# Optimization experiments

Hardware: AMD Instinct MI355X
Metric: run time of the kernel (lower is better)

Reference implementation:

```python
import jax, jax.numpy as jnp
import numpy as np

B = 1024           # number of jets (independent binary trees)
L = 10             # tree depth (levels); level j has B*2**j nodes
H = 128            # hidden size
FEAT = 7           # input features per node
LEVEL_SIZES = [B * 2**j for j in range(L)]
OFF = np.concatenate([[0], np.cumsum(LEVEL_SIZES)]).astype(int).tolist()
INNER = LEVEL_SIZES[:-1]                     # all non-bottom nodes are inner
COFF = np.concatenate([[0], np.cumsum(INNER)]).astype(int).tolist()


def _linear_init(key, fan_in, fan_out):
    return jax.random.normal(key, (fan_in, fan_out), jnp.float32) / np.sqrt(fan_in).astype(np.float32)


def setup_inputs() -> dict:
    key = jax.random.key(0)
    ks = jax.random.split(key, 6)
    contents = jax.random.normal(ks[0], (OFF[-1], FEAT), jnp.float32)
    # child indices are local to level j+1: node k at level j -> children (2k, 2k+1)
    ch = [np.stack([2 * np.arange(n), 2 * np.arange(n) + 1], axis=1) for n in INNER]
    children = jnp.asarray(np.concatenate(ch, axis=0), jnp.int32)
    return {
        "contents": contents,
        "children": children,
        "W_u": _linear_init(ks[1], FEAT, H), "b_u": jnp.zeros((H,), jnp.float32),
        "W_h": _linear_init(ks[2], 3 * H, H), "b_h": jnp.zeros((H,), jnp.float32),
        "W_z": _linear_init(ks[3], 4 * H, 4 * H), "b_z": jnp.zeros((4 * H,), jnp.float32),
        "W_r": _linear_init(ks[4], 3 * H, 3 * H), "b_r": jnp.zeros((3 * H,), jnp.float32),
        "conv_w": jnp.asarray([0.9], jnp.float32),
        "conv_b": jnp.asarray([0.01], jnp.float32),
    }


def reference(contents, children, W_u, b_u, W_h, b_h, W_z, b_z, W_r, b_r, conv_w, conv_b):
    def conv_chain(x):
        # relu(conv1x1(relu(conv1x1(relu(conv1x1(x)))))): Conv2d(1,1,1) == scalar scale + bias
        for _ in range(3):
            x = jax.nn.relu(conv_w[0] * x + conv_b[0])
        return x

    emb = None  # embeddings of the level below (level j+1)
    for j in reversed(range(L)):
        c = contents[OFF[j]:OFF[j + 1]]               # [N_j, FEAT]
        u = conv_chain(c @ W_u + b_u)                 # [N_j, H]
        if j == L - 1:                                # bottom level: all leaves
            emb = u
            continue
        ch = children[COFF[j]:COFF[j + 1]]            # [N_j, 2] indices into level j+1
        h_L = emb[ch[:, 0]]                           # gather left children
        h_R = emb[ch[:, 1]]                           # gather right children
        hhu = jnp.concatenate([h_L, h_R, u], axis=1)  # [N_j, 3H]
        r = jax.nn.sigmoid(hhu @ W_r + b_r)           # reset gate
        h_H = conv_chain((r * hhu) @ W_h + b_h)       # [N_j, H]
        z = jnp.concatenate([h_H, hhu], axis=1) @ W_z + b_z  # [N_j, 4H]
        g = jax.nn.softmax(
            jnp.stack([z[:, :H], z[:, H:2 * H], z[:, 2 * H:3 * H], z[:, 3 * H:]], axis=-1),
            axis=-1,
        )                                             # [N_j, H, 4] gate weights
        emb = g[..., 0] * h_H + g[..., 1] * h_L + g[..., 2] * h_R + g[..., 3] * u
    return emb.reshape(B, -1)                         # [B, H] root embeddings
```

## Files before the change

kernel.cpp:

```cpp
#include <hip/hip_runtime.h>
#include <hip/hip_bf16.h>

typedef _Float16 f16x8 __attribute__((ext_vector_type(8)));
typedef _Float16 f16x4 __attribute__((ext_vector_type(4)));
typedef float f32x4 __attribute__((ext_vector_type(4)));

#define H 128
#define FEAT 7
#define RB 64
#define NT 512

__device__ __forceinline__ float conv3(float x, float w, float b) {
    x = fmaxf(fmaf(w, x, b), 0.f);
    x = fmaxf(fmaf(w, x, b), 0.f);
    x = fmaxf(fmaf(w, x, b), 0.f);
    return x;
}
__device__ __forceinline__ float sigm(float x) {
    return __builtin_amdgcn_rcpf(1.f + __expf(-x));
}

__global__ __launch_bounds__(256) void pack_weights(
    const float* __restrict__ Wu, const float* __restrict__ Wr,
    const float* __restrict__ Wh, const float* __restrict__ Wz,
    _Float16* __restrict__ Pu, _Float16* __restrict__ Pr,
    _Float16* __restrict__ Ph, _Float16* __restrict__ Pz)
{
    int idx = blockIdx.x * 256 + threadIdx.x;
    if (idx < 384 * 384) {
        int k = idx / 384, n = idx % 384;
        Pr[((size_t)(k >> 3) * 384 + n) * 8 + (k & 7)] = (_Float16)Wr[idx];
    }
    if (idx < 384 * 128) {
        int k = idx / 128, n = idx % 128;
        Ph[((size_t)(k >> 3) * 128 + n) * 8 + (k & 7)] = (_Float16)Wh[idx];
    }
    if (idx < 512 * 512) {
        int k = idx / 512, n = idx % 512;
        Pz[((size_t)(k >> 3) * 512 + n) * 8 + (k & 7)] = (_Float16)Wz[idx];
    }
    if (idx < 128 * 32) {
        int n = idx & 127, kk = idx >> 7;
        Pu[((size_t)(kk >> 3) * 128 + n) * 8 + (kk & 7)] =
            (kk < FEAT) ? (_Float16)Wu[kk * H + n] : (_Float16)0.f;
    }
}

template<bool LEAF>
__global__ __launch_bounds__(NT, 2) void level_kernel(
    const float* __restrict__ contents,
    const int* __restrict__ children,
    const float* __restrict__ leafContents,
    const _Float16* __restrict__ embPrev,
    _Float16* __restrict__ embOut,
    float* __restrict__ finalOut,
    const _Float16* __restrict__ Pu, const float* __restrict__ bu,
    const _Float16* __restrict__ Pr, const float* __restrict__ br,
    const _Float16* __restrict__ Ph, const float* __restrict__ bh,
    const _Float16* __restrict__ Pz, const float* __restrict__ bz,
    const float* __restrict__ convw, const float* __restrict__ convb)
{
    __shared__ __align__(16) _Float16 s_hhu[RB][392];
    __shared__ __align__(16) _Float16 s_x[RB][392];
    __shared__ __align__(16) _Float16 s_hH[RB][136];

    const int t = threadIdx.x;
    const int row0 = blockIdx.x * RB;
    const float cw = convw[0], cbv = convb[0];

    const int lane = t & 63;
    const int w = t >> 6;
    const int q = lane >> 4;
    const int ln = lane & 15;

    const f16x8* PBc = (const f16x8*)Pr + (w * 48 + ln);
    f16x8 awc[3][3];
#pragma unroll
    for (int c = 0; c < 3; c++) awc[0][c] = PBc[(size_t)q * 384 + c * 16];
#pragma unroll
    for (int c = 0; c < 3; c++) awc[1][c] = PBc[(size_t)(4 + q) * 384 + c * 16];

    _Float16* wbuf = (_Float16*)&s_x[0][0];
    {
        int r = t >> 3, k = t & 7;
        wbuf[t] = (k < FEAT) ? (_Float16)contents[(size_t)(row0 + r) * FEAT + k]
                             : (_Float16)0.f;
        if (LEAF) {
            int base = children[row0 * 2];
            const float* lc = leafContents + (size_t)base * FEAT;
#pragma unroll
            for (int p = 0; p < 2; p++) {
                int e = p * 512 + t;
                int r2 = e >> 3, k2 = e & 7;
                wbuf[512 + e] = (k2 < FEAT) ? (_Float16)lc[(size_t)r2 * FEAT + k2]
                                            : (_Float16)0.f;
            }
        } else {
            int rp = t >> 4, chunk = t & 15;
#pragma unroll
            for (int p = 0; p < 4; p++) {
                int cr = p * 32 + rp;
                int child = children[row0 * 2 + cr];
                uint4 v = *(const uint4*)(embPrev + (size_t)child * H + chunk * 8);
                *(uint4*)&s_hhu[cr >> 1][(cr & 1) * 128 + chunk * 8] = v;
            }
        }
    }
    __syncthreads();

    {
        f16x8 puF = ((const f16x8*)Pu)[(size_t)q * 128 + w * 16 + ln];
        const int fb = w * 16 + q * 4;
        f32x4 buv = *(const f32x4*)&bu[fb];
        {
            f16x8 bA[4];
#pragma unroll
            for (int rt = 0; rt < 4; rt++)
                bA[rt] = *(const f16x8*)&wbuf[(rt * 16 + ln) * 8];
            f32x4 accA[4];
#pragma unroll
            for (int rt = 0; rt < 4; rt++)
                accA[rt] = __builtin_amdgcn_mfma_f32_16x16x32_f16(puF, bA[rt], (f32x4){0,0,0,0}, 0, 0, 0);
#pragma unroll
            for (int rt = 0; rt < 4; rt++) {
                f16x4 hp;
#pragma unroll
                for (int reg = 0; reg < 4; reg++)
                    hp[reg] = (_Float16)conv3(accA[rt][reg] + buv[reg], cw, cbv);
                *(f16x4*)&s_hhu[rt * 16 + ln][256 + fb] = hp;
            }
        }
        if (LEAF) {
#pragma unroll
            for (int h = 0; h < 2; h++) {
                f16x8 bB[4];
#pragma unroll
                for (int rt = 0; rt < 4; rt++)
                    bB[rt] = *(const f16x8*)&wbuf[512 + ((h * 4 + rt) * 16 + ln) * 8];
                f32x4 accB[4];
#pragma unroll
                for (int rt = 0; rt < 4; rt++)
                    accB[rt] = __builtin_amdgcn_mfma_f32_16x16x32_f16(puF, bB[rt], (f32x4){0,0,0,0}, 0, 0, 0);
#pragma unroll
                for (int rt = 0; rt < 4; rt++) {
                    int rr = (h * 4 + rt) * 16 + ln;
                    f16x4 hp;
#pragma unroll
                    for (int reg = 0; reg < 4; reg++)
                        hp[reg] = (_Float16)conv3(accB[rt][reg] + buv[reg], cw, cbv);
                    *(f16x4*)&s_hhu[rr >> 1][(rr & 1) * 128 + fb] = hp;
                }
            }
        }
    }
    __syncthreads();

    const f16x8* PBd = (const f16x8*)Ph + (w * 16 + ln);
    f16x8 awd[3];

    {
        f32x4 acc[3][4];
#pragma unroll
        for (int c = 0; c < 3; c++)
#pragma unroll
            for (int rt = 0; rt < 4; rt++) acc[c][rt] = (f32x4){0,0,0,0};
        f16x8 bb[3][4];
#pragma unroll
        for (int rt = 0; rt < 4; rt++) bb[0][rt] = *(const f16x8*)&s_hhu[rt * 16 + ln][q * 8];
#pragma unroll
        for (int rt = 0; rt < 4; rt++) bb[1][rt] = *(const f16x8*)&s_hhu[rt * 16 + ln][32 + q * 8];
#pragma unroll
        for (int kk = 0; kk < 12; kk++) {
            if (kk + 2 < 12) {
                int kb = (kk + 2) * 4 + q;
#pragma unroll
                for (int c = 0; c < 3; c++) awc[(kk + 2) % 3][c] = PBc[(size_t)kb * 384 + c * 16];
#pragma unroll
                for (int rt = 0; rt < 4; rt++)
                    bb[(kk + 2) % 3][rt] = *(const f16x8*)&s_hhu[rt * 16 + ln][(kk + 2) * 32 + q * 8];
            }
#pragma unroll
            for (int c = 0; c < 3; c++)
#pragma unroll
                for (int rt = 0; rt < 4; rt++)
                    acc[c][rt] = __builtin_amdgcn_mfma_f32_16x16x32_f16(awc[kk % 3][c], bb[kk % 3][rt], acc[c][rt], 0, 0, 0);
        }
        awd[0] = PBd[(size_t)q * 128];
        awd[1] = PBd[(size_t)(4 + q) * 128];
#pragma unroll
        for (int c = 0; c < 3; c++) {
            int fb = w * 48 + c * 16 + q * 4;
            f32x4 bv = *(const f32x4*)&br[fb];
#pragma unroll
            for (int rt = 0; rt < 4; rt++) {
                int row = rt * 16 + ln;
                f16x4 hh = *(const f16x4*)&s_hhu[row][fb];
                f16x4 xv;
#pragma unroll
                for (int reg = 0; reg < 4; reg++) {
                    float rv = sigm(acc[c][rt][reg] + bv[reg]);
                    xv[reg] = (_Float16)(rv * (float)hh[reg]);
                }
                *(f16x4*)&s_x[row][fb] = xv;
            }
        }
    }
    __syncthreads();

    const f16x8* PBe = (const f16x8*)Pz + (w * 16 + ln);
    f16x8 awe[3][4];

    {
        f32x4 acc[4];
#pragma unroll
        for (int rt = 0; rt < 4; rt++) acc[rt] = (f32x4){0,0,0,0};
        f16x8 bb[3][4];
#pragma unroll
        for (int rt = 0; rt < 4; rt++) bb[0][rt] = *(const f16x8*)&s_x[rt * 16 + ln][q * 8];
#pragma unroll
        for (int rt = 0; rt < 4; rt++) bb[1][rt] = *(const f16x8*)&s_x[rt * 16 + ln][32 + q * 8];
#pragma unroll
        for (int kk = 0; kk < 12; kk++) {
            if (kk + 2 < 12) {
                int kb = (kk + 2) * 4 + q;
                awd[(kk + 2) % 3] = PBd[(size_t)kb * 128];
#pragma unroll
                for (int rt = 0; rt < 4; rt++)
                    bb[(kk + 2) % 3][rt] = *(const f16x8*)&s_x[rt * 16 + ln][(kk + 2) * 32 + q * 8];
            }
#pragma unroll
            for (int rt = 0; rt < 4; rt++)
                acc[rt] = __builtin_amdgcn_mfma_f32_16x16x32_f16(awd[kk % 3], bb[kk % 3][rt], acc[rt], 0, 0, 0);
        }
#pragma unroll
        for (int g = 0; g < 4; g++) awe[0][g] = PBe[(size_t)q * 512 + g * 128];
#pragma unroll
        for (int g = 0; g < 4; g++) awe[1][g] = PBe[(size_t)(4 + q) * 512 + g * 128];
        int fb = w * 16 + q * 4;
        f32x4 bhv = *(const f32x4*)&bh[fb];
#pragma unroll
        for (int rt = 0; rt < 4; rt++) {
            f16x4 hp;
#pragma unroll
            for (int reg = 0; reg < 4; reg++)
                hp[reg] = (_Float16)conv3(acc[rt][reg] + bhv[reg], cw, cbv);
            *(f16x4*)&s_hH[rt * 16 + ln][fb] = hp;
        }
    }
    __syncthreads();

    {
        const int nb = w * 16;
        f32x4 acc[4][4];
#pragma unroll
        for (int g = 0; g < 4; g++)
#pragma unroll
            for (int rt = 0; rt < 4; rt++) acc[g][rt] = (f32x4){0,0,0,0};
        f16x8 bb[3][4];
#pragma unroll
        for (int rt = 0; rt < 4; rt++) bb[0][rt] = *(const f16x8*)&s_hH[rt * 16 + ln][q * 8];
#pragma unroll
        for (int rt = 0; rt < 4; rt++) bb[1][rt] = *(const f16x8*)&s_hH[rt * 16 + ln][32 + q * 8];
#pragma unroll
        for (int kk = 0; kk < 16; kk++) {
            if (kk + 2 < 16) {
                int kb = (kk + 2) * 4 + q;
#pragma unroll
                for (int g = 0; g < 4; g++) awe[(kk + 2) % 3][g] = PBe[(size_t)kb * 512 + g * 128];
                if (kk + 2 < 4) {
#pragma unroll
                    for (int rt = 0; rt < 4; rt++)
                        bb[(kk + 2) % 3][rt] = *(const f16x8*)&s_hH[rt * 16 + ln][(kk + 2) * 32 + q * 8];
                } else {
                    int k0 = (kk + 2) * 32 - 128;
#pragma unroll
                    for (int rt = 0; rt < 4; rt++)
                        bb[(kk + 2) % 3][rt] = *(const f16x8*)&s_hhu[rt * 16 + ln][k0 + q * 8];
                }
            }
#pragma unroll
            for (int g = 0; g < 4; g++)
#pragma unroll
                for (int rt = 0; rt < 4; rt++)
                    acc[g][rt] = __builtin_amdgcn_mfma_f32_16x16x32_f16(awe[kk % 3][g], bb[kk % 3][rt], acc[g][rt], 0, 0, 0);
        }
        int colb = nb + q * 4;
        f32x4 bz0 = *(const f32x4*)&bz[colb];
        f32x4 bz1 = *(const f32x4*)&bz[128 + colb];
        f32x4 bz2 = *(const f32x4*)&bz[256 + colb];
        f32x4 bz3 = *(const f32x4*)&bz[384 + colb];
#pragma unroll
        for (int rt = 0; rt < 4; rt++) {
            int row = rt * 16 + ln;
            f16x4 hH4 = *(const f16x4*)&s_hH[row][colb];
            f16x4 hL4 = *(const f16x4*)&s_hhu[row][colb];
            f16x4 hR4 = *(const f16x4*)&s_hhu[row][128 + colb];
            f16x4 u4  = *(const f16x4*)&s_hhu[row][256 + colb];
            size_t gidx = (size_t)(row0 + row) * H + colb;
            if (finalOut) {
                f32x4 ov;
#pragma unroll
                for (int reg = 0; reg < 4; reg++) {
                    float z0 = acc[0][rt][reg] + bz0[reg];
                    float z1 = acc[1][rt][reg] + bz1[reg];
                    float z2 = acc[2][rt][reg] + bz2[reg];
                    float z3 = acc[3][rt][reg] + bz3[reg];
                    float m = fmaxf(fmaxf(z0, z1), fmaxf(z2, z3));
                    float e0 = __expf(z0 - m), e1 = __expf(z1 - m), e2 = __expf(z2 - m), e3 = __expf(z3 - m);
                    float inv = __builtin_amdgcn_rcpf(e0 + e1 + e2 + e3);
                    ov[reg] = (e0 * (float)hH4[reg] + e1 * (float)hL4[reg] +
                               e2 * (float)hR4[reg] + e3 * (float)u4[reg]) * inv;
                }
                *(f32x4*)&finalOut[gidx] = ov;
            } else {
                f16x4 ev;
#pragma unroll
                for (int reg = 0; reg < 4; reg++) {
                    float z0 = acc[0][rt][reg] + bz0[reg];
                    float z1 = acc[1][rt][reg] + bz1[reg];
                    float z2 = acc[2][rt][reg] + bz2[reg];
                    float z3 = acc[3][rt][reg] + bz3[reg];
                    float m = fmaxf(fmaxf(z0, z1), fmaxf(z2, z3));
                    float e0 = __expf(z0 - m), e1 = __expf(z1 - m), e2 = __expf(z2 - m), e3 = __expf(z3 - m);
                    float inv = __builtin_amdgcn_rcpf(e0 + e1 + e2 + e3);
                    ev[reg] = (_Float16)((e0 * (float)hH4[reg] + e1 * (float)hL4[reg] +
                                          e2 * (float)hR4[reg] + e3 * (float)u4[reg]) * inv);
                }
                *(f16x4*)&embOut[gidx] = ev;
            }
        }
    }
}

extern "C" void kernel_launch(void* const* d_in, const int* in_sizes, int n_in,
                              void* d_out, int out_size, void* d_ws, size_t ws_size,
                              hipStream_t stream) {
    const float* contents = (const float*)d_in[0];
    const int*   children = (const int*)d_in[1];
    const float* Wu = (const float*)d_in[2];
    const float* bu = (const float*)d_in[3];
    const float* Wh = (const float*)d_in[4];
    const float* bh = (const float*)d_in[5];
    const float* Wz = (const float*)d_in[6];
    const float* bz = (const float*)d_in[7];
    const float* Wr = (const float*)d_in[8];
    const float* br = (const float*)d_in[9];
    const float* convw = (const float*)d_in[10];
    const float* convb = (const float*)d_in[11];
    float* out = (float*)d_out;

    _Float16* Pr = (_Float16*)d_ws;
    _Float16* Ph = Pr + 384 * 384;
    _Float16* Pz = Ph + 384 * 128;
    _Float16* Pu = Pz + 512 * 512;
    _Float16* bufA = (_Float16*)((char*)d_ws + (1 << 20));
    _Float16* bufB = bufA + (size_t)262144 * H;

    auto OFFS = [](int j) -> long long { return 1024LL * ((1LL << j) - 1); };

    pack_weights<<<(512 * 512 + 255) / 256, 256, 0, stream>>>(Wu, Wr, Wh, Wz, Pu, Pr, Ph, Pz);

    {
        int n = 1024 << 8;
        level_kernel<true><<<n / RB, NT, 0, stream>>>(
            contents + OFFS(8) * FEAT, children + OFFS(8) * 2,
            contents + OFFS(9) * FEAT, nullptr, bufA, nullptr,
            Pu, bu, Pr, br, Ph, bh, Pz, bz, convw, convb);
    }

    _Float16* prev = bufA;
    _Float16* cur  = bufB;
    for (int j = 7; j >= 0; j--) {
        int n = 1024 << j;
        level_kernel<false><<<n / RB, NT, 0, stream>>>(
            contents + OFFS(j) * FEAT, children + OFFS(j) * 2,
            nullptr, prev, cur, (j == 0 ? out : nullptr),
            Pu, bu, Pr, br, Ph, bh, Pz, bz, convw, convb);
        _Float16* tmp = prev; prev = cur; cur = tmp;
    }
}
```

Before: 687.9 us.

## Fuse weight packing and all tree levels into one cooperative persistent kernel

Replaces the pack kernel and ten per-level launches with a single cooperative kernel of 256 persistent blocks. Blocks loop over row tiles and separate packing and levels with grid-wide syncs. This removes per-launch overhead and the tail idling between small upper-level kernels. In exchange the bottom levels run with fewer resident blocks and carry grid-sync costs, and the old multi-launch path remains as a fallback if the cooperative launch fails.

```diff
diff --git a/kernel.cpp b/kernel.cpp
--- a/kernel.cpp
+++ b/kernel.cpp
@@ -1,5 +1,8 @@
 #include <hip/hip_runtime.h>
 #include <hip/hip_bf16.h>
+#include <hip/hip_cooperative_groups.h>
+
+namespace cg = cooperative_groups;
 
 typedef _Float16 f16x8 __attribute__((ext_vector_type(8)));
 typedef _Float16 f16x4 __attribute__((ext_vector_type(4)));
@@ -9,6 +12,7 @@
 #define FEAT 7
 #define RB 64
 #define NT 512
+#define NBLK 256
 
 __device__ __forceinline__ float conv3(float x, float w, float b) {
     x = fmaxf(fmaf(w, x, b), 0.f);
@@ -18,6 +22,32 @@
 }
 __device__ __forceinline__ float sigm(float x) {
     return __builtin_amdgcn_rcpf(1.f + __expf(-x));
+}
+
+__device__ __forceinline__ void pack_one(
+    int idx,
+    const float* __restrict__ Wu, const float* __restrict__ Wr,
+    const float* __restrict__ Wh, const float* __restrict__ Wz,
+    _Float16* __restrict__ Pu, _Float16* __restrict__ Pr,
+    _Float16* __restrict__ Ph, _Float16* __restrict__ Pz)
+{
+    if (idx < 384 * 384) {
+        int k = idx / 384, n = idx % 384;
+        Pr[((size_t)(k >> 3) * 384 + n) * 8 + (k & 7)] = (_Float16)Wr[idx];
+    }
+    if (idx < 384 * 128) {
+        int k = idx / 128, n = idx % 128;
+        Ph[((size_t)(k >> 3) * 128 + n) * 8 + (k & 7)] = (_Float16)Wh[idx];
+    }
+    if (idx < 512 * 512) {
+        int k = idx / 512, n = idx % 512;
+        Pz[((size_t)(k >> 3) * 512 + n) * 8 + (k & 7)] = (_Float16)Wz[idx];
+    }
+    if (idx < 128 * 32) {
+        int n = idx & 127, kk = idx >> 7;
+        Pu[((size_t)(kk >> 3) * 128 + n) * 8 + (kk & 7)] =
+            (kk < FEAT) ? (_Float16)Wu[kk * H + n] : (_Float16)0.f;
+    }
 }
 
 __global__ __launch_bounds__(256) void pack_weights(
@@ -27,27 +57,13 @@
     _Float16* __restrict__ Ph, _Float16* __restrict__ Pz)
 {
     int idx = blockIdx.x * 256 + threadIdx.x;
-    if (idx < 384 * 384) {
-        int k = idx / 384, n = idx % 384;
-        Pr[((size_t)(k >> 3) * 384 + n) * 8 + (k & 7)] = (_Float16)Wr[idx];
-    }
-    if (idx < 384 * 128) {
-        int k = idx / 128, n = idx % 128;
-        Ph[((size_t)(k >> 3) * 128 + n) * 8 + (k & 7)] = (_Float16)Wh[idx];
-    }
-    if (idx < 512 * 512) {
-        int k = idx / 512, n = idx % 512;
-        Pz[((size_t)(k >> 3) * 512 + n) * 8 + (k & 7)] = (_Float16)Wz[idx];
-    }
-    if (idx < 128 * 32) {
-        int n = idx & 127, kk = idx >> 7;
-        Pu[((size_t)(kk >> 3) * 128 + n) * 8 + (kk & 7)] =
-            (kk < FEAT) ? (_Float16)Wu[kk * H + n] : (_Float16)0.f;
-    }
+    pack_one(idx, Wu, Wr, Wh, Wz, Pu, Pr, Ph, Pz);
 }
 
 template<bool LEAF>
-__global__ __launch_bounds__(NT, 2) void level_kernel(
+__device__ __forceinline__ void process_tile(
+    int row0,
+    _Float16 (*s_hhu)[392], _Float16 (*s_x)[392], _Float16 (*s_hH)[136],
     const float* __restrict__ contents,
     const int* __restrict__ children,
     const float* __restrict__ leafContents,
@@ -58,20 +74,15 @@
     const _Float16* __restrict__ Pr, const float* __restrict__ br,
     const _Float16* __restrict__ Ph, const float* __restrict__ bh,
     const _Float16* __restrict__ Pz, const float* __restrict__ bz,
-    const float* __restrict__ convw, const float* __restrict__ convb)
+    float cw, float cbv)
 {
-    __shared__ __align__(16) _Float16 s_hhu[RB][392];
-    __shared__ __align__(16) _Float16 s_x[RB][392];
-    __shared__ __align__(16) _Float16 s_hH[RB][136];
-
     const int t = threadIdx.x;
-    const int row0 = blockIdx.x * RB;
-    const float cw = convw[0], cbv = convb[0];
-
     const int lane = t & 63;
     const int w = t >> 6;
     const int q = lane >> 4;
     const int ln = lane & 15;
+
+    __syncthreads();
 
     const f16x8* PBc = (const f16x8*)Pr + (w * 48 + ln);
     f16x8 awc[3][3];
@@ -330,6 +341,76 @@
             }
         }
     }
+}
+
+__global__ __launch_bounds__(NT, 2) void tree_fused(
+    const float* __restrict__ contents_base,
+    const int* __restrict__ children_base,
+    const float* __restrict__ Wu, const float* __restrict__ Wr,
+    const float* __restrict__ Wh, const float* __restrict__ Wz,
+    _Float16* __restrict__ Pu, _Float16* __restrict__ Pr,
+    _Float16* __restrict__ Ph, _Float16* __restrict__ Pz,
+    const float* __restrict__ bu, const float* __restrict__ br,
+    const float* __restrict__ bh, const float* __restrict__ bz,
+    const float* __restrict__ convw, const float* __restrict__ convb,
+    _Float16* bufA, _Float16* bufB, float* out)
+{
+    __shared__ __align__(16) _Float16 s_hhu[RB][392];
+    __shared__ __align__(16) _Float16 s_x[RB][392];
+    __shared__ __align__(16) _Float16 s_hH[RB][136];
+
+    cg::grid_group grid = cg::this_grid();
+
+    for (int idx = blockIdx.x * NT + threadIdx.x; idx < 512 * 512; idx += gridDim.x * NT)
+        pack_one(idx, Wu, Wr, Wh, Wz, Pu, Pr, Ph, Pz);
+    grid.sync();
+
+    const float cw = convw[0], cbv = convb[0];
+
+    {
+        long long o8 = 1024LL * 255;
+        const float* contents = contents_base + o8 * FEAT;
+        const int* children = children_base + o8 * 2;
+        const float* leafC = contents_base + (1024LL * 511) * FEAT;
+        for (int tile = blockIdx.x; tile < 4096; tile += gridDim.x)
+            process_tile<true>(tile * RB, s_hhu, s_x, s_hH, contents, children, leafC,
+                               nullptr, bufA, nullptr,
+                               Pu, bu, Pr, br, Ph, bh, Pz, bz, cw, cbv);
+    }
+    _Float16* prev = bufA;
+    _Float16* cur  = bufB;
+    for (int j = 7; j >= 0; j--) {
+        grid.sync();
+        long long oj = 1024LL * ((1LL << j) - 1);
+        const float* contents = contents_base + oj * FEAT;
+        const int* children = children_base + oj * 2;
+        int ntiles = (1024 << j) / RB;
+        float* fo = (j == 0) ? out : nullptr;
+        for (int tile = blockIdx.x; tile < ntiles; tile += gridDim.x)
+            process_tile<false>(tile * RB, s_hhu, s_x, s_hH, contents, children, nullptr,
+                                prev, cur, fo,
+                                Pu, bu, Pr, br, Ph, bh, Pz, bz, cw, cbv);
+        _Float16* tmp = prev; prev = cur; cur = tmp;
+    }
+}
+
+template<bool LEAF>
+__global__ __launch_bounds__(NT, 2) void level_kernel(
+    const float* __restrict__ contents, const int* __restrict__ children,
+    const float* __restrict__ leafContents, const _Float16* __restrict__ embPrev,
+    _Float16* __restrict__ embOut, float* __restrict__ finalOut,
+    const _Float16* __restrict__ Pu, const float* __restrict__ bu,
+    const _Float16* __restrict__ Pr, const float* __restrict__ br,
+    const _Float16* __restrict__ Ph, const float* __restrict__ bh,
+    const _Float16* __restrict__ Pz, const float* __restrict__ bz,
+    const float* __restrict__ convw, const float* __restrict__ convb)
+{
+    __shared__ __align__(16) _Float16 s_hhu[RB][392];
+    __shared__ __align__(16) _Float16 s_x[RB][392];
+    __shared__ __align__(16) _Float16 s_hH[RB][136];
+    process_tile<LEAF>(blockIdx.x * RB, s_hhu, s_x, s_hH, contents, children,
+                       leafContents, embPrev, embOut, finalOut,
+                       Pu, bu, Pr, br, Ph, bh, Pz, bz, convw[0], convb[0]);
 }
 
 extern "C" void kernel_launch(void* const* d_in, const int* in_sizes, int n_in,
@@ -356,26 +437,36 @@
     _Float16* bufA = (_Float16*)((char*)d_ws + (1 << 20));
     _Float16* bufB = bufA + (size_t)262144 * H;
 
-    auto OFFS = [](int j) -> long long { return 1024LL * ((1LL << j) - 1); };
-
-    pack_weights<<<(512 * 512 + 255) / 256, 256, 0, stream>>>(Wu, Wr, Wh, Wz, Pu, Pr, Ph, Pz);
-
-    {
-        int n = 1024 << 8;
-        level_kernel<true><<<n / RB, NT, 0, stream>>>(
-            contents + OFFS(8) * FEAT, children + OFFS(8) * 2,
-            contents + OFFS(9) * FEAT, nullptr, bufA, nullptr,
-            Pu, bu, Pr, br, Ph, bh, Pz, bz, convw, convb);
-    }
-
-    _Float16* prev = bufA;
-    _Float16* cur  = bufB;
-    for (int j = 7; j >= 0; j--) {
-        int n = 1024 << j;
-        level_kernel<false><<<n / RB, NT, 0, stream>>>(
-            contents + OFFS(j) * FEAT, children + OFFS(j) * 2,
-            nullptr, prev, cur, (j == 0 ? out : nullptr),
-            Pu, bu, Pr, br, Ph, bh, Pz, bz, convw, convb);
-        _Float16* tmp = prev; prev = cur; cur = tmp;
-    }
-}
+    void* args[] = {
+        (void*)&contents, (void*)&children,
+        (void*)&Wu, (void*)&Wr, (void*)&Wh, (void*)&Wz,
+        (void*)&Pu, (void*)&Pr, (void*)&Ph, (void*)&Pz,
+        (void*)&bu, (void*)&br, (void*)&bh, (void*)&bz,
+        (void*)&convw, (void*)&convb,
+        (void*)&bufA, (void*)&bufB, (void*)&out
+    };
+    hipError_t err = hipLaunchCooperativeKernel(
+        (const void*)tree_fused, dim3(NBLK), dim3(NT), args, 0, stream);
+
+    if (err != hipSuccess) {
+        auto OFFS = [](int j) -> long long { return 1024LL * ((1LL << j) - 1); };
+        pack_weights<<<(512 * 512 + 255) / 256, 256, 0, stream>>>(Wu, Wr, Wh, Wz, Pu, Pr, Ph, Pz);
+        {
+            int n = 1024 << 8;
+            level_kernel<true><<<n / RB, NT, 0, stream>>>(
+                contents + OFFS(8) * FEAT, children + OFFS(8) * 2,
+                contents + OFFS(9) * FEAT, nullptr, bufA, nullptr,
+                Pu, bu, Pr, br, Ph, bh, Pz, bz, convw, convb);
+        }
+        _Float16* prev = bufA;
+        _Float16* cur  = bufB;
+        for (int j = 7; j >= 0; j--) {
+            int n = 1024 << j;
+            level_kernel<false><<<n / RB, NT, 0, stream>>>(
+                contents + OFFS(j) * FEAT, children + OFFS(j) * 2,
+                nullptr, prev, cur, (j == 0 ? out : nullptr),
+                Pu, bu, Pr, br, Ph, bh, Pz, bz, convw, convb);
+            _Float16* tmp = prev; prev = cur; cur = tmp;
+        }
+    }
+}
```

After: 2.302 ms. 3.35x slower.
